# Optimization experiments

Measured on AMD Instinct MI355X. Metric: run time of the kernel, lower is better.

Reference implementation:

```python
import jax, jax.numpy as jnp
import numpy as np


def setup_inputs() -> dict:
    key = jax.random.key(0)
    k_u, k_wl, k_b, k_c = jax.random.split(key, 4)
    B_, T, D, N = 4, 4096, 1024, 256
    u = jax.random.normal(k_u, (B_, T, D), dtype=jnp.float32)
    # torch init: W_lambda.weight zeros, bias 2.0; B, C xavier_uniform gain=0.5.
    # Use small random weights for W_lambda too so the path is exercised.
    Wl = jax.random.normal(k_wl, (N, D), dtype=jnp.float32) * 0.02
    bl = jnp.full((N,), 2.0, dtype=jnp.float32)
    xav_b = 0.5 * np.sqrt(6.0 / (D + N))
    Wb = jax.random.uniform(k_b, (N, D), dtype=jnp.float32, minval=-xav_b, maxval=xav_b)
    xav_c = 0.5 * np.sqrt(6.0 / (N + D))
    Wc = jax.random.uniform(k_c, (D, N), dtype=jnp.float32, minval=-xav_c, maxval=xav_c)
    Dp = jnp.zeros((D,), dtype=jnp.float32)
    return {"u": u, "Wl": Wl, "bl": bl, "Wb": Wb, "Wc": Wc, "Dp": Dp}


def reference(u, Wl, bl, Wb, Wc, Dp):
    # u: (B, T, D). Precompute per-step gates and inputs with batched GEMMs,
    # then run the diagonal linear recurrence with lax.scan over time.
    lam = jax.nn.sigmoid(jnp.einsum('btd,nd->btn', u, Wl) + bl)  # (B, T, N)
    Bu = jnp.einsum('btd,nd->btn', u, Wb)                         # (B, T, N)

    def step(h, inp):
        lam_t, bu_t = inp            # each (B, N)
        h = lam_t * h + bu_t
        return h, h

    h0 = jnp.zeros((u.shape[0], Wl.shape[0]), dtype=u.dtype)
    # scan over time: move T to leading axis
    _, H = jax.lax.scan(step, h0, (jnp.swapaxes(lam, 0, 1), jnp.swapaxes(Bu, 0, 1)))
    H = jnp.swapaxes(H, 0, 1)        # (B, T, N)
    y = jnp.einsum('btn,dn->btd', H, Wc) + u * Dp
    return y
```

## Files before the change

### kernel.cpp

```cpp
#include <hip/hip_runtime.h>


typedef __bf16 bf16_t;
typedef __attribute__((ext_vector_type(8))) __bf16 bf16x8;
typedef __attribute__((ext_vector_type(4))) __bf16 bf16x4;
typedef __attribute__((ext_vector_type(4))) float f32x4;

#define B_  4
#define T_  4096
#define D_  1024
#define N_  256
#define BT  (B_ * T_)
#define NCHUNK 128
#define CHLEN  (T_ / NCHUNK)

#define GLOAD_LDS16(g, l) __builtin_amdgcn_global_load_lds(              \
    (__attribute__((address_space(1))) void*)(g),                        \
    (__attribute__((address_space(3))) void*)(l), 16, 0, 0)

__global__ void cvt_weights(const float* __restrict__ Wl,
                            const float* __restrict__ Wb,
                            const float* __restrict__ Wc,
                            bf16_t* __restrict__ Wcomb,
                            bf16_t* __restrict__ Wc_bf) {
  int i = blockIdx.x * 256 + threadIdx.x;
  if (i < 131072) {
    int e = i * 4;
    int j = e >> 10;
    int d = e & 1023;
    const float* src = (j < 256) ? (Wl + (size_t)j * D_ + d)
                                 : (Wb + (size_t)(j - 256) * D_ + d);
    float4 v = *(const float4*)src;
    bf16x4 o = {(__bf16)v.x, (__bf16)v.y, (__bf16)v.z, (__bf16)v.w};
    ((bf16x4*)Wcomb)[i] = o;
  } else {
    int k = i - 131072;
    float4 v = ((const float4*)Wc)[k];
    bf16x4 o = {(__bf16)v.x, (__bf16)v.y, (__bf16)v.z, (__bf16)v.w};
    ((bf16x4*)Wc_bf)[k] = o;
  }
}

__device__ __forceinline__ void mfma_tile8(const bf16_t* bufA, const bf16_t* bufB,
                                           int wr, int wc, int r16, int kq,
                                           f32x4 (&acc)[4][2]) {
  const int sw = (r16 & 7) << 3;
#pragma unroll
  for (int kk = 0; kk < 2; ++kk) {
    bf16x8 af[4], bfr[2];
#pragma unroll
    for (int m = 0; m < 4; ++m) {
      int idx = (wr * 64 + m * 16 + r16) * 64 + kk * 32 + kq * 8;
      af[m] = *(const bf16x8*)&bufA[idx ^ sw];
    }
#pragma unroll
    for (int n = 0; n < 2; ++n) {
      int idx = (wc * 32 + n * 16 + r16) * 64 + kk * 32 + kq * 8;
      bfr[n] = *(const bf16x8*)&bufB[idx ^ sw];
    }
#pragma unroll
    for (int m = 0; m < 4; ++m)
#pragma unroll
      for (int n = 0; n < 2; ++n)
        acc[m][n] = __builtin_amdgcn_mfma_f32_16x16x32_bf16(af[m], bfr[n], acc[m][n], 0, 0, 0);
  }
}

__global__ __launch_bounds__(512, 4)
void gemm1_kernel(const float* __restrict__ A, const bf16_t* __restrict__ Bm,
                  bf16_t* __restrict__ Lam, bf16_t* __restrict__ Bu,
                  const float* __restrict__ bl) {
  __shared__ bf16_t lA[2][128 * 64];
  __shared__ bf16_t lB[2][128 * 64];
  const int wid  = threadIdx.x >> 6;
  const int lane = threadIdx.x & 63;
  const int work = (blockIdx.x & 7) * 64 + (blockIdx.x >> 3);
  const int brow = work >> 2;
  const int bcol = work & 3;
  const int r16 = lane & 15;
  const int kq  = lane >> 4;
  const int wr = wid >> 2, wc = wid & 3;

  f32x4 acc[4][2] = {};

  const int ar = lane >> 4;
  const int ac = (lane & 15) * 4;
  const float* gA = A + (size_t)(brow * 128 + wid * 16 + ar) * D_ + ac;
  const int aw_base = (wid * 16 + ar) * 64 + ac;

  const bf16_t* gB = Bm + (size_t)(bcol * 128 + wid * 16 + (lane >> 3)) * D_
                        + (size_t)(((lane & 7) ^ (lane >> 3)) * 8);

  {
    float4 va[4];
#pragma unroll
    for (int i = 0; i < 4; ++i)
      va[i] = *(const float4*)(gA + (size_t)(i * 4) * D_);
#pragma unroll
    for (int i = 0; i < 2; ++i)
      GLOAD_LDS16(gB + (size_t)(i * 8) * D_, &lB[0][(wid * 16 + i * 8) * 64]);
#pragma unroll
    for (int i = 0; i < 4; ++i) {
      bf16x4 o = {(__bf16)va[i].x, (__bf16)va[i].y,
                  (__bf16)va[i].z, (__bf16)va[i].w};
      int idx = (aw_base + i * 4 * 64) ^ (((ar + 4 * (i & 1)) & 7) << 3);
      *(bf16x4*)&lA[0][idx] = o;
    }
    __syncthreads();
  }

  int cur = 0;
#pragma unroll 1
  for (int k0 = 0; k0 < D_ - 64; k0 += 64) {
    float4 va[4];
#pragma unroll
    for (int i = 0; i < 4; ++i)
      va[i] = *(const float4*)(gA + (size_t)(i * 4) * D_ + k0 + 64);
#pragma unroll
    for (int i = 0; i < 2; ++i)
      GLOAD_LDS16(gB + (size_t)(i * 8) * D_ + k0 + 64,
                  &lB[cur ^ 1][(wid * 16 + i * 8) * 64]);
    mfma_tile8(lA[cur], lB[cur], wr, wc, r16, kq, acc);
#pragma unroll
    for (int i = 0; i < 4; ++i) {
      bf16x4 o = {(__bf16)va[i].x, (__bf16)va[i].y,
                  (__bf16)va[i].z, (__bf16)va[i].w};
      int idx = (aw_base + i * 4 * 64) ^ (((ar + 4 * (i & 1)) & 7) << 3);
      *(bf16x4*)&lA[cur ^ 1][idx] = o;
    }
    __syncthreads();
    cur ^= 1;
  }
  mfma_tile8(lA[cur], lB[cur], wr, wc, r16, kq, acc);

#pragma unroll
  for (int m = 0; m < 4; ++m) {
#pragma unroll
    for (int n = 0; n < 2; ++n) {
      int row0 = brow * 128 + wr * 64 + m * 16 + kq * 4;
      int col  = bcol * 128 + wc * 32 + n * 16 + r16;
#pragma unroll
      for (int j = 0; j < 4; ++j) {
        float v = acc[m][n][j];
        int row = row0 + j;
        if (bcol < 2) {
          v = 1.0f / (1.0f + __expf(-(v + bl[col])));
          Lam[(size_t)row * N_ + col] = (__bf16)v;
        } else {
          Bu[(size_t)row * N_ + (col - 256)] = (__bf16)v;
        }
      }
    }
  }
}

__global__ __launch_bounds__(512, 4)
void gemm2_kernel(const bf16_t* __restrict__ A, const bf16_t* __restrict__ Bm,
                  float* __restrict__ C,
                  const float* __restrict__ u, const float* __restrict__ Dp) {
  __shared__ bf16_t lA[2][128 * 64];
  __shared__ bf16_t lB[2][128 * 64];
  const int wid  = threadIdx.x >> 6;
  const int lane = threadIdx.x & 63;
  const int brow = blockIdx.x;
  const int bcol = blockIdx.y;
  const int r16 = lane & 15;
  const int kq  = lane >> 4;
  const int wr = wid >> 2, wc = wid & 3;

  f32x4 acc[4][2] = {};

  const size_t scol = ((lane & 7) ^ (lane >> 3)) * 8;
  const bf16_t* gA = A + (size_t)(brow * 128 + wid * 16 + (lane >> 3)) * N_ + scol;
  const bf16_t* gB = Bm + (size_t)(bcol * 128 + wid * 16 + (lane >> 3)) * N_ + scol;

  {
#pragma unroll
    for (int i = 0; i < 2; ++i) {
      GLOAD_LDS16(gA + (size_t)(i * 8) * N_, &lA[0][(wid * 16 + i * 8) * 64]);
      GLOAD_LDS16(gB + (size_t)(i * 8) * N_, &lB[0][(wid * 16 + i * 8) * 64]);
    }
    __syncthreads();
  }
  int cur = 0;
#pragma unroll 1
  for (int k0 = 0; k0 < N_ - 64; k0 += 64) {
#pragma unroll
    for (int i = 0; i < 2; ++i) {
      GLOAD_LDS16(gA + (size_t)(i * 8) * N_ + k0 + 64,
                  &lA[cur ^ 1][(wid * 16 + i * 8) * 64]);
      GLOAD_LDS16(gB + (size_t)(i * 8) * N_ + k0 + 64,
                  &lB[cur ^ 1][(wid * 16 + i * 8) * 64]);
    }
    mfma_tile8(lA[cur], lB[cur], wr, wc, r16, kq, acc);
    __syncthreads();
    cur ^= 1;
  }
  mfma_tile8(lA[cur], lB[cur], wr, wc, r16, kq, acc);

#pragma unroll
  for (int m = 0; m < 4; ++m) {
#pragma unroll
    for (int n = 0; n < 2; ++n) {
      int row0 = brow * 128 + wr * 64 + m * 16 + kq * 4;
      int col  = bcol * 128 + wc * 32 + n * 16 + r16;
#pragma unroll
      for (int j = 0; j < 4; ++j) {
        int row = row0 + j;
        float v = acc[m][n][j] + Dp[col] * u[(size_t)row * D_ + col];
        C[(size_t)row * D_ + col] = v;
      }
    }
  }
}

__global__ __launch_bounds__(64)
void scan_phase1(const bf16_t* __restrict__ Lam, const bf16_t* __restrict__ Bu,
                 float* __restrict__ wsA, float* __restrict__ wsB) {
  int tid = blockIdx.x * 64 + threadIdx.x;
  int ng = tid & 31;
  int chunk = (tid >> 5) & (NCHUNK - 1);
  int b = tid >> 12;
  size_t base = ((size_t)(b * T_ + chunk * CHLEN)) * N_ + ng * 8;
  float A[8], h[8];
#pragma unroll
  for (int i = 0; i < 8; ++i) { A[i] = 1.f; h[i] = 0.f; }
#pragma unroll 8
  for (int t = 0; t < CHLEN; ++t) {
    bf16x8 lv = *(const bf16x8*)&Lam[base + (size_t)t * N_];
    bf16x8 bv = *(const bf16x8*)&Bu[base + (size_t)t * N_];
#pragma unroll
    for (int i = 0; i < 8; ++i) {
      float l = (float)lv[i];
      A[i] *= l;
      h[i] = fmaf(l, h[i], (float)bv[i]);
    }
  }
  size_t o = ((size_t)(b * NCHUNK + chunk)) * N_ + ng * 8;
#pragma unroll
  for (int i = 0; i < 8; ++i) { wsA[o + i] = A[i]; wsB[o + i] = h[i]; }
}

__global__ void scan_phase2(const float* __restrict__ wsA,
                            const float* __restrict__ wsB,
                            float* __restrict__ carry) {
  int tid = blockIdx.x * 256 + threadIdx.x;
  int n = tid & 255;
  int b = tid >> 8;
  float h = 0.f;
#pragma unroll 8
  for (int c = 0; c < NCHUNK; ++c) {
    size_t idx = ((size_t)(b * NCHUNK + c)) * N_ + n;
    carry[idx] = h;
    h = fmaf(wsA[idx], h, wsB[idx]);
  }
}

__global__ __launch_bounds__(64)
void scan_phase3(const bf16_t* __restrict__ Lam, const bf16_t* __restrict__ Bu,
                 const float* __restrict__ carry, bf16_t* __restrict__ H) {
  int tid = blockIdx.x * 64 + threadIdx.x;
  int ng = tid & 31;
  int chunk = (tid >> 5) & (NCHUNK - 1);
  int b = tid >> 12;
  size_t base = ((size_t)(b * T_ + chunk * CHLEN)) * N_ + ng * 8;
  size_t o = ((size_t)(b * NCHUNK + chunk)) * N_ + ng * 8;
  float h[8];
#pragma unroll
  for (int i = 0; i < 8; ++i) h[i] = carry[o + i];
#pragma unroll 8
  for (int t = 0; t < CHLEN; ++t) {
    bf16x8 lv = *(const bf16x8*)&Lam[base + (size_t)t * N_];
    bf16x8 bv = *(const bf16x8*)&Bu[base + (size_t)t * N_];
    bf16x8 hv;
#pragma unroll
    for (int i = 0; i < 8; ++i) {
      h[i] = fmaf((float)lv[i], h[i], (float)bv[i]);
      hv[i] = (__bf16)h[i];
    }
    *(bf16x8*)&H[base + (size_t)t * N_] = hv;
  }
}

extern "C" void kernel_launch(void* const* d_in, const int* in_sizes, int n_in,
                              void* d_out, int out_size, void* d_ws, size_t ws_size,
                              hipStream_t stream) {
  const float* u  = (const float*)d_in[0];
  const float* Wl = (const float*)d_in[1];
  const float* bl = (const float*)d_in[2];
  const float* Wb = (const float*)d_in[3];
  const float* Wc = (const float*)d_in[4];
  const float* Dp = (const float*)d_in[5];
  float* y = (float*)d_out;

  char* ws = (char*)d_ws;
  bf16_t* Lam   = (bf16_t*)(ws + 0);
  bf16_t* Bu    = (bf16_t*)(ws + 8388608);
  bf16_t* H     = (bf16_t*)(ws + 16777216);
  bf16_t* Wcomb = (bf16_t*)(ws + 25165824);
  bf16_t* Wc_bf = (bf16_t*)(ws + 26214400);
  float*  wsA   = (float*)(ws + 26738688);
  float*  wsB   = (float*)(ws + 27262976);
  float*  carry = (float*)(ws + 27787264);

  cvt_weights<<<768, 256, 0, stream>>>(Wl, Wb, Wc, Wcomb, Wc_bf);

  gemm1_kernel<<<512, 512, 0, stream>>>(u, Wcomb, Lam, Bu, bl);

  scan_phase1<<<256, 64, 0, stream>>>(Lam, Bu, wsA, wsB);
  scan_phase2<<<4, 256, 0, stream>>>(wsA, wsB, carry);
  scan_phase3<<<256, 64, 0, stream>>>(Lam, Bu, carry, H);

  dim3 g2(BT / 128, D_ / 128);
  gemm2_kernel<<<g2, 512, 0, stream>>>(H, Wc_bf, y, u, Dp);
}
```

Before: 206.2 us.

## Stage GEMM epilogues through LDS, skip zero Dp term, double scan chunks

Both GEMM epilogues now write accumulators to a padded LDS tile and then issue coalesced vector stores (bf16x8 for Lam/Bu, f32x4 for y), replacing scattered scalar stores. The gemm2 epilogue checks with a wave ballot whether any Dp value is nonzero and skips reading u when all are zero. The scan uses 256 chunks of length 16 with 256-thread blocks and fully unrolled inner loops, so more threads run in parallel in phases 1 and 3 while the sequential phase 2 gets longer. The larger shared-memory footprint (about 66 KB) may reduce occupancy.

```diff
diff --git a/kernel.cpp b/kernel.cpp
--- a/kernel.cpp
+++ b/kernel.cpp
@@ -11,8 +11,9 @@
 #define D_  1024
 #define N_  256
 #define BT  (B_ * T_)
-#define NCHUNK 128
+#define NCHUNK 256
 #define CHLEN  (T_ / NCHUNK)
+#define FSTRIDE 132
 
 #define GLOAD_LDS16(g, l) __builtin_amdgcn_global_load_lds(              \
     (__attribute__((address_space(1))) void*)(g),                        \
@@ -66,12 +67,28 @@
   }
 }
 
+__device__ __forceinline__ void acc_to_lds(float* ft, int wr, int wc,
+                                           int r16, int kq,
+                                           const f32x4 (&acc)[4][2]) {
+#pragma unroll
+  for (int m = 0; m < 4; ++m)
+#pragma unroll
+    for (int n = 0; n < 2; ++n)
+#pragma unroll
+      for (int j = 0; j < 4; ++j) {
+        int rl = wr * 64 + m * 16 + kq * 4 + j;
+        int cl = wc * 32 + n * 16 + r16;
+        ft[rl * FSTRIDE + cl] = acc[m][n][j];
+      }
+}
+
 __global__ __launch_bounds__(512, 4)
 void gemm1_kernel(const float* __restrict__ A, const bf16_t* __restrict__ Bm,
                   bf16_t* __restrict__ Lam, bf16_t* __restrict__ Bu,
                   const float* __restrict__ bl) {
-  __shared__ bf16_t lA[2][128 * 64];
-  __shared__ bf16_t lB[2][128 * 64];
+  __shared__ char smem[128 * FSTRIDE * 4];
+  bf16_t* lA = (bf16_t*)smem;
+  bf16_t* lB = (bf16_t*)(smem + 32768);
   const int wid  = threadIdx.x >> 6;
   const int lane = threadIdx.x & 63;
   const int work = (blockIdx.x & 7) * 64 + (blockIdx.x >> 3);
@@ -98,13 +115,13 @@
       va[i] = *(const float4*)(gA + (size_t)(i * 4) * D_);
 #pragma unroll
     for (int i = 0; i < 2; ++i)
-      GLOAD_LDS16(gB + (size_t)(i * 8) * D_, &lB[0][(wid * 16 + i * 8) * 64]);
+      GLOAD_LDS16(gB + (size_t)(i * 8) * D_, &lB[(wid * 16 + i * 8) * 64]);
 #pragma unroll
     for (int i = 0; i < 4; ++i) {
       bf16x4 o = {(__bf16)va[i].x, (__bf16)va[i].y,
                   (__bf16)va[i].z, (__bf16)va[i].w};
       int idx = (aw_base + i * 4 * 64) ^ (((ar + 4 * (i & 1)) & 7) << 3);
-      *(bf16x4*)&lA[0][idx] = o;
+      *(bf16x4*)&lA[idx] = o;
     }
     __syncthreads();
   }
@@ -119,37 +136,49 @@
 #pragma unroll
     for (int i = 0; i < 2; ++i)
       GLOAD_LDS16(gB + (size_t)(i * 8) * D_ + k0 + 64,
-                  &lB[cur ^ 1][(wid * 16 + i * 8) * 64]);
-    mfma_tile8(lA[cur], lB[cur], wr, wc, r16, kq, acc);
+                  &lB[(cur ^ 1) * 8192 + (wid * 16 + i * 8) * 64]);
+    mfma_tile8(&lA[cur * 8192], &lB[cur * 8192], wr, wc, r16, kq, acc);
 #pragma unroll
     for (int i = 0; i < 4; ++i) {
       bf16x4 o = {(__bf16)va[i].x, (__bf16)va[i].y,
                   (__bf16)va[i].z, (__bf16)va[i].w};
       int idx = (aw_base + i * 4 * 64) ^ (((ar + 4 * (i & 1)) & 7) << 3);
-      *(bf16x4*)&lA[cur ^ 1][idx] = o;
+      *(bf16x4*)&lA[(cur ^ 1) * 8192 + idx] = o;
     }
     __syncthreads();
     cur ^= 1;
   }
-  mfma_tile8(lA[cur], lB[cur], wr, wc, r16, kq, acc);
-
-#pragma unroll
-  for (int m = 0; m < 4; ++m) {
-#pragma unroll
-    for (int n = 0; n < 2; ++n) {
-      int row0 = brow * 128 + wr * 64 + m * 16 + kq * 4;
-      int col  = bcol * 128 + wc * 32 + n * 16 + r16;
-#pragma unroll
-      for (int j = 0; j < 4; ++j) {
-        float v = acc[m][n][j];
-        int row = row0 + j;
-        if (bcol < 2) {
-          v = 1.0f / (1.0f + __expf(-(v + bl[col])));
-          Lam[(size_t)row * N_ + col] = (__bf16)v;
-        } else {
-          Bu[(size_t)row * N_ + (col - 256)] = (__bf16)v;
-        }
+  mfma_tile8(&lA[cur * 8192], &lB[cur * 8192], wr, wc, r16, kq, acc);
+
+  __syncthreads();
+  float* ft = (float*)smem;
+  acc_to_lds(ft, wr, wc, r16, kq, acc);
+  __syncthreads();
+  const int tr = threadIdx.x >> 4;
+  const int tc = (threadIdx.x & 15) * 8;
+#pragma unroll
+  for (int p = 0; p < 4; ++p) {
+    int rl = p * 32 + tr;
+    int row = brow * 128 + rl;
+    f32x4 a = *(f32x4*)&ft[rl * FSTRIDE + tc];
+    f32x4 b = *(f32x4*)&ft[rl * FSTRIDE + tc + 4];
+    bf16x8 o;
+    if (bcol < 2) {
+      int colg = bcol * 128 + tc;
+#pragma unroll
+      for (int q = 0; q < 4; ++q) {
+        o[q]     = (__bf16)(1.0f / (1.0f + __expf(-(a[q] + bl[colg + q]))));
+        o[q + 4] = (__bf16)(1.0f / (1.0f + __expf(-(b[q] + bl[colg + 4 + q]))));
       }
+      *(bf16x8*)&Lam[(size_t)row * N_ + colg] = o;
+    } else {
+      int colg = (bcol - 2) * 128 + tc;
+#pragma unroll
+      for (int q = 0; q < 4; ++q) {
+        o[q] = (__bf16)a[q];
+        o[q + 4] = (__bf16)b[q];
+      }
+      *(bf16x8*)&Bu[(size_t)row * N_ + colg] = o;
     }
   }
 }
@@ -158,8 +187,9 @@
 void gemm2_kernel(const bf16_t* __restrict__ A, const bf16_t* __restrict__ Bm,
                   float* __restrict__ C,
                   const float* __restrict__ u, const float* __restrict__ Dp) {
-  __shared__ bf16_t lA[2][128 * 64];
-  __shared__ bf16_t lB[2][128 * 64];
+  __shared__ char smem[128 * FSTRIDE * 4];
+  bf16_t* lA = (bf16_t*)smem;
+  bf16_t* lB = (bf16_t*)(smem + 32768);
   const int wid  = threadIdx.x >> 6;
   const int lane = threadIdx.x & 63;
   const int brow = blockIdx.x;
@@ -177,8 +207,8 @@
   {
 #pragma unroll
     for (int i = 0; i < 2; ++i) {
-      GLOAD_LDS16(gA + (size_t)(i * 8) * N_, &lA[0][(wid * 16 + i * 8) * 64]);
-      GLOAD_LDS16(gB + (size_t)(i * 8) * N_, &lB[0][(wid * 16 + i * 8) * 64]);
+      GLOAD_LDS16(gA + (size_t)(i * 8) * N_, &lA[(wid * 16 + i * 8) * 64]);
+      GLOAD_LDS16(gB + (size_t)(i * 8) * N_, &lB[(wid * 16 + i * 8) * 64]);
     }
     __syncthreads();
   }
@@ -188,44 +218,52 @@
 #pragma unroll
     for (int i = 0; i < 2; ++i) {
       GLOAD_LDS16(gA + (size_t)(i * 8) * N_ + k0 + 64,
-                  &lA[cur ^ 1][(wid * 16 + i * 8) * 64]);
+                  &lA[(cur ^ 1) * 8192 + (wid * 16 + i * 8) * 64]);
       GLOAD_LDS16(gB + (size_t)(i * 8) * N_ + k0 + 64,
-                  &lB[cur ^ 1][(wid * 16 + i * 8) * 64]);
-    }
-    mfma_tile8(lA[cur], lB[cur], wr, wc, r16, kq, acc);
+                  &lB[(cur ^ 1) * 8192 + (wid * 16 + i * 8) * 64]);
+    }
+    mfma_tile8(&lA[cur * 8192], &lB[cur * 8192], wr, wc, r16, kq, acc);
     __syncthreads();
     cur ^= 1;
   }
-  mfma_tile8(lA[cur], lB[cur], wr, wc, r16, kq, acc);
-
-#pragma unroll
-  for (int m = 0; m < 4; ++m) {
-#pragma unroll
-    for (int n = 0; n < 2; ++n) {
-      int row0 = brow * 128 + wr * 64 + m * 16 + kq * 4;
-      int col  = bcol * 128 + wc * 32 + n * 16 + r16;
-#pragma unroll
-      for (int j = 0; j < 4; ++j) {
-        int row = row0 + j;
-        float v = acc[m][n][j] + Dp[col] * u[(size_t)row * D_ + col];
-        C[(size_t)row * D_ + col] = v;
-      }
-    }
-  }
-}
-
-__global__ __launch_bounds__(64)
+  mfma_tile8(&lA[cur * 8192], &lB[cur * 8192], wr, wc, r16, kq, acc);
+
+  __syncthreads();
+  float* ft = (float*)smem;
+  acc_to_lds(ft, wr, wc, r16, kq, acc);
+  __syncthreads();
+  const int tr = threadIdx.x >> 5;
+  const int tc = (threadIdx.x & 31) * 4;
+  const int colg = bcol * 128 + tc;
+  f32x4 dp = *(const f32x4*)&Dp[colg];
+  bool need = (dp[0] != 0.f) | (dp[1] != 0.f) | (dp[2] != 0.f) | (dp[3] != 0.f);
+  unsigned long long anyd = __ballot(need);
+#pragma unroll
+  for (int p = 0; p < 8; ++p) {
+    int rl = p * 16 + tr;
+    int row = brow * 128 + rl;
+    f32x4 v = *(f32x4*)&ft[rl * FSTRIDE + tc];
+    if (anyd) {
+      f32x4 uv = *(const f32x4*)&u[(size_t)row * D_ + colg];
+#pragma unroll
+      for (int q = 0; q < 4; ++q) v[q] = fmaf(dp[q], uv[q], v[q]);
+    }
+    *(f32x4*)&C[(size_t)row * D_ + colg] = v;
+  }
+}
+
+__global__ __launch_bounds__(256)
 void scan_phase1(const bf16_t* __restrict__ Lam, const bf16_t* __restrict__ Bu,
                  float* __restrict__ wsA, float* __restrict__ wsB) {
-  int tid = blockIdx.x * 64 + threadIdx.x;
+  int tid = blockIdx.x * 256 + threadIdx.x;
   int ng = tid & 31;
   int chunk = (tid >> 5) & (NCHUNK - 1);
-  int b = tid >> 12;
+  int b = tid >> 13;
   size_t base = ((size_t)(b * T_ + chunk * CHLEN)) * N_ + ng * 8;
   float A[8], h[8];
 #pragma unroll
   for (int i = 0; i < 8; ++i) { A[i] = 1.f; h[i] = 0.f; }
-#pragma unroll 8
+#pragma unroll
   for (int t = 0; t < CHLEN; ++t) {
     bf16x8 lv = *(const bf16x8*)&Lam[base + (size_t)t * N_];
     bf16x8 bv = *(const bf16x8*)&Bu[base + (size_t)t * N_];
@@ -256,19 +294,19 @@
   }
 }
 
-__global__ __launch_bounds__(64)
+__global__ __launch_bounds__(256)
 void scan_phase3(const bf16_t* __restrict__ Lam, const bf16_t* __restrict__ Bu,
                  const float* __restrict__ carry, bf16_t* __restrict__ H) {
-  int tid = blockIdx.x * 64 + threadIdx.x;
+  int tid = blockIdx.x * 256 + threadIdx.x;
   int ng = tid & 31;
   int chunk = (tid >> 5) & (NCHUNK - 1);
-  int b = tid >> 12;
+  int b = tid >> 13;
   size_t base = ((size_t)(b * T_ + chunk * CHLEN)) * N_ + ng * 8;
   size_t o = ((size_t)(b * NCHUNK + chunk)) * N_ + ng * 8;
   float h[8];
 #pragma unroll
   for (int i = 0; i < 8; ++i) h[i] = carry[o + i];
-#pragma unroll 8
+#pragma unroll
   for (int t = 0; t < CHLEN; ++t) {
     bf16x8 lv = *(const bf16x8*)&Lam[base + (size_t)t * N_];
     bf16x8 bv = *(const bf16x8*)&Bu[base + (size_t)t * N_];
@@ -300,16 +338,16 @@
   bf16_t* Wcomb = (bf16_t*)(ws + 25165824);
   bf16_t* Wc_bf = (bf16_t*)(ws + 26214400);
   float*  wsA   = (float*)(ws + 26738688);
-  float*  wsB   = (float*)(ws + 27262976);
-  float*  carry = (float*)(ws + 27787264);
+  float*  wsB   = (float*)(ws + 27787264);
+  float*  carry = (float*)(ws + 28835840);
 
   cvt_weights<<<768, 256, 0, stream>>>(Wl, Wb, Wc, Wcomb, Wc_bf);
 
   gemm1_kernel<<<512, 512, 0, stream>>>(u, Wcomb, Lam, Bu, bl);
 
-  scan_phase1<<<256, 64, 0, stream>>>(Lam, Bu, wsA, wsB);
+  scan_phase1<<<128, 256, 0, stream>>>(Lam, Bu, wsA, wsB);
   scan_phase2<<<4, 256, 0, stream>>>(wsA, wsB, carry);
-  scan_phase3<<<256, 64, 0, stream>>>(Lam, Bu, carry, H);
+  scan_phase3<<<128, 256, 0, stream>>>(Lam, Bu, carry, H);
 
   dim3 g2(BT / 128, D_ / 128);
   gemm2_kernel<<<g2, 512, 0, stream>>>(H, Wc_bf, y, u, Dp);
```

After: 201.1 us. 1.03x faster.
